# Optimization experiments

Measured on AMD Instinct MI355X. Metric: run time of the kernel, lower is better.

Reference implementation:

```python
import jax, jax.numpy as jnp
import numpy as np

D = 1024  # feature dim, power of two
B = 8192  # batch


def build_H(d):
    # scaled Hadamard matrix H with H @ H = I (since H is symmetric orthogonal)
    H = np.array([[1.0]], dtype=np.float32)
    while H.shape[0] < d:
        H = np.block([[H, H], [H, -H]])
    return jnp.asarray(H * d ** -0.5, dtype=jnp.float32)


def setup_inputs() -> dict:
    key = jax.random.key(0)
    ks = jax.random.split(key, 6)
    return {
        "x": jax.random.normal(ks[0], (B, D), jnp.float32),
        "s1": jax.random.normal(ks[1], (D,), jnp.float32),
        "s2": jax.random.normal(ks[2], (D,), jnp.float32),
        "mu": jax.random.normal(ks[3], (D,), jnp.float32),
        "Rho": jax.random.normal(ks[4], (D, D), jnp.float32),
        "epsilon": jax.random.normal(ks[5], (D,), jnp.float32),  # torch.randn(D) noise, hoisted
        "H": build_H(D),
    }


def _w_bar(s1, s2, u, H):
    # diag(s1) @ H @ diag(u) @ H @ diag(s2), via row/col scalings of H
    return ((s1[:, None] * H * u[None, :]) @ H) * s2[None, :]


def reference(x, s1, s2, mu, Rho, epsilon, H):
    r = jax.nn.softplus(Rho)
    sigma_sqrt = r @ r.T                      # [D, D]
    # w_bar is linear in u, so w_bar(mu) @ h + w_bar(sigma_sqrt @ eps) @ h
    # == w_bar(mu + sigma_sqrt @ eps) @ h  (same math, one GEMM chain)
    u = mu + sigma_sqrt @ epsilon             # [D]
    W = _w_bar(s1, s2, u, H)                  # [D, D]
    b = W @ x.T                               # [D, B]  (h = x.T as in the torch code)
    return jax.nn.relu(b)
```

## Files before the change

### kernel.cpp

```cpp
#include <hip/hip_runtime.h>
#include <math.h>

#define DD 1024
#define BB 8192

__device__ __forceinline__ float softplus_f(float x) {
    return fmaxf(x, 0.0f) + log1pf(expf(-fabsf(x)));
}

__global__ __launch_bounds__(256) void k_teps(const float* __restrict__ rho,
                                              const float* __restrict__ eps,
                                              float* __restrict__ t) {
    int j  = blockIdx.x * 256 + threadIdx.x;
    int i0 = blockIdx.y * 16;
    float acc = 0.f;
#pragma unroll
    for (int k = 0; k < 16; ++k) {
        int i = i0 + k;
        acc += softplus_f(rho[i * DD + j]) * eps[i];
    }
    atomicAdd(&t[j], acc);
}

__global__ __launch_bounds__(256) void k_u(const float* __restrict__ rho,
                                           const float* __restrict__ mu,
                                           const float* __restrict__ t,
                                           float* __restrict__ u) {
    int i  = blockIdx.x;
    int tx = threadIdx.x;
    float acc = 0.f;
#pragma unroll
    for (int c = 0; c < 4; ++c) {
        int j = tx + c * 256;
        acc += softplus_f(rho[i * DD + j]) * t[j];
    }
#pragma unroll
    for (int off = 32; off > 0; off >>= 1)
        acc += __shfl_down(acc, off, 64);
    __shared__ float red[4];
    int lane = tx & 63, w = tx >> 6;
    if (lane == 0) red[w] = acc;
    __syncthreads();
    if (tx == 0) u[i] = mu[i] + red[0] + red[1] + red[2] + red[3];
}


template <int CTRL>
__device__ __forceinline__ float dppmov(float x) {
    return __int_as_float(
        __builtin_amdgcn_mov_dpp(__float_as_int(x), CTRL, 0xF, 0xF, true));
}

__device__ __forceinline__ void fwht1024(float v[16], float sA, float sB,
                                         float sC, float sD, float sE, float sF) {
#pragma unroll
    for (int s = 1; s <= 8; s <<= 1) {
#pragma unroll
        for (int m = 0; m < 16; ++m)
            if ((m & s) == 0) {
                float a = v[m], b = v[m ^ s];
                v[m] = a + b;
                v[m ^ s] = a - b;
            }
    }
#pragma unroll
    for (int m = 0; m < 16; ++m) { float o = dppmov<0xB1>(v[m]);  v[m] = fmaf(v[m], sA, o); }
#pragma unroll
    for (int m = 0; m < 16; ++m) { float o = dppmov<0x4E>(v[m]);  v[m] = fmaf(v[m], sB, o); }
#pragma unroll
    for (int m = 0; m < 16; ++m) { float o = dppmov<0x141>(v[m]); v[m] = fmaf(v[m], sC, o); }
#pragma unroll
    for (int m = 0; m < 16; ++m) { float o = dppmov<0x140>(v[m]); v[m] = fmaf(v[m], sD, o); }
#pragma unroll
    for (int m = 0; m < 16; ++m) { float o = __shfl_xor(v[m], 16, 64); v[m] = fmaf(v[m], sE, o); }
#pragma unroll
    for (int m = 0; m < 16; ++m) { float o = __shfl_xor(v[m], 32, 64); v[m] = fmaf(v[m], sF, o); }
}

__global__ __launch_bounds__(512) void k_main(const float* __restrict__ x,
                                              const float* __restrict__ s1,
                                              const float* __restrict__ s2,
                                              const float* __restrict__ u,
                                              float* __restrict__ out) {
    __shared__ float tile[16 * 1024];
    const int t    = threadIdx.x;
    const int lane = t & 63;
    const int wv   = t >> 6;
    const int b0   = blockIdx.x * 16;

    const int l0 = lane & 1, l1 = (lane >> 1) & 1, l2 = (lane >> 2) & 1,
              l3 = (lane >> 3) & 1, l4 = (lane >> 4) & 1, l5 = (lane >> 5) & 1;
    const int hi = (l0 ^ l2) | ((l1 ^ l2) << 1) | ((l2 ^ l3) << 2) | (l3 << 3) |
                   (l4 << 4) | (l5 << 5);
    const int base = hi << 4;

    const float sA = (l0 ^ l2) ? -1.f : 1.f;
    const float sB = (l1 ^ l2) ? -1.f : 1.f;
    const float sC = (l2 ^ l3) ? -1.f : 1.f;
    const float sD = l3 ? -1.f : 1.f;
    const float sE = l4 ? -1.f : 1.f;
    const float sF = l5 ? -1.f : 1.f;

    float4 s2f[4], uf[4], s1f[4];
#pragma unroll
    for (int c = 0; c < 4; ++c) {
        s2f[c] = *(const float4*)(s2 + base + 4 * c);
        uf[c]  = *(const float4*)(u  + base + 4 * c);
        s1f[c] = *(const float4*)(s1 + base + 4 * c);
    }
    const int swz = (lane >> 1) & 15;

    for (int rr = 0; rr < 2; ++rr) {
        const int r = wv * 2 + rr;
        const float* xr = x + (b0 + r) * DD + base;
        float v[16];
#pragma unroll
        for (int c = 0; c < 4; ++c) {
            float4 xv = *(const float4*)(xr + 4 * c);
            v[4 * c + 0] = xv.x * s2f[c].x;
            v[4 * c + 1] = xv.y * s2f[c].y;
            v[4 * c + 2] = xv.z * s2f[c].z;
            v[4 * c + 3] = xv.w * s2f[c].w;
        }
        fwht1024(v, sA, sB, sC, sD, sE, sF);
#pragma unroll
        for (int c = 0; c < 4; ++c) {
            v[4 * c + 0] *= uf[c].x;
            v[4 * c + 1] *= uf[c].y;
            v[4 * c + 2] *= uf[c].z;
            v[4 * c + 3] *= uf[c].w;
        }
        fwht1024(v, sA, sB, sC, sD, sE, sF);
        const float kscale = 1.0f / 1024.0f;
        float* trow = tile + r * 1024 + base;
        const int sw2 = (swz ^ r) & 15;
#pragma unroll
        for (int c = 0; c < 4; ++c) {
            float y0 = fmaxf(v[4 * c + 0] * s1f[c].x * kscale, 0.f);
            float y1 = fmaxf(v[4 * c + 1] * s1f[c].y * kscale, 0.f);
            float y2 = fmaxf(v[4 * c + 2] * s1f[c].z * kscale, 0.f);
            float y3 = fmaxf(v[4 * c + 3] * s1f[c].w * kscale, 0.f);
            trow[(4 * c + 0) ^ sw2] = y0;
            trow[(4 * c + 1) ^ sw2] = y1;
            trow[(4 * c + 2) ^ sw2] = y2;
            trow[(4 * c + 3) ^ sw2] = y3;
        }
    }
    __syncthreads();

#pragma unroll
    for (int it = 0; it < 32; ++it) {
        int d = (t >> 4) + (it << 5);
        int r = t & 15;
        int h  = d >> 4;
        int h1 = (h >> 1) & 1, h2 = (h >> 2) & 1, h3 = (h >> 3) & 1,
            h4 = (h >> 4) & 1;
        int sw = (h1 ^ h2 ^ h3) | ((h2 ^ h3) << 1) | (h3 << 2) | (h4 << 3);
        float y = tile[r * 1024 + (d & ~15) + (((d & 15) ^ sw ^ r) & 15)];
        out[d * BB + b0 + r] = y;
    }
}

extern "C" void kernel_launch(void* const* d_in, const int* in_sizes, int n_in,
                              void* d_out, int out_size, void* d_ws, size_t ws_size,
                              hipStream_t stream) {
    const float* x   = (const float*)d_in[0];
    const float* s1  = (const float*)d_in[1];
    const float* s2  = (const float*)d_in[2];
    const float* mu  = (const float*)d_in[3];
    const float* rho = (const float*)d_in[4];
    const float* eps = (const float*)d_in[5];
    float* out = (float*)d_out;

    float* t = (float*)d_ws;
    float* u = t + DD;

    hipMemsetAsync(t, 0, DD * sizeof(float), stream);

    dim3 gA(4, 64);
    k_teps<<<gA, 256, 0, stream>>>(rho, eps, t);
    k_u<<<DD, 256, 0, stream>>>(rho, mu, t, u);
    k_main<<<BB / 16, 512, 0, stream>>>(x, s1, s2, u, out);
}
```

Baseline: 37.55 us.

## Vectorize transposed output stores, preload both rows, and drop atomics in t reduction

The transposed write-out now has each thread gather four batch rows from shared memory and emit one float4 store, replacing the scalar stores. The shared-tile layout gets an extra row-dependent XOR on the column block to keep bank conflicts down. Both rows' x loads are issued up front, and the 1/1024 scale is folded into s1. The t = softplus(Rho)^T eps step becomes a per-column block reduction with no memset and no atomics. That reduction reads Rho with a stride of one row per thread, which is uncoalesced and could make the small kernel slower.

```diff
diff --git a/kernel.cpp b/kernel.cpp
--- a/kernel.cpp
+++ b/kernel.cpp
@@ -8,18 +8,25 @@
     return fmaxf(x, 0.0f) + log1pf(expf(-fabsf(x)));
 }
 
-__global__ __launch_bounds__(256) void k_teps(const float* __restrict__ rho,
-                                              const float* __restrict__ eps,
-                                              float* __restrict__ t) {
-    int j  = blockIdx.x * 256 + threadIdx.x;
-    int i0 = blockIdx.y * 16;
+__global__ __launch_bounds__(256) void k_t(const float* __restrict__ rho,
+                                           const float* __restrict__ eps,
+                                           float* __restrict__ t) {
+    int j  = blockIdx.x;
+    int tx = threadIdx.x;
     float acc = 0.f;
 #pragma unroll
-    for (int k = 0; k < 16; ++k) {
-        int i = i0 + k;
+    for (int c = 0; c < 4; ++c) {
+        int i = tx + c * 256;
         acc += softplus_f(rho[i * DD + j]) * eps[i];
     }
-    atomicAdd(&t[j], acc);
+#pragma unroll
+    for (int off = 32; off > 0; off >>= 1)
+        acc += __shfl_down(acc, off, 64);
+    __shared__ float red[4];
+    int lane = tx & 63, w = tx >> 6;
+    if (lane == 0) red[w] = acc;
+    __syncthreads();
+    if (tx == 0) t[j] = red[0] + red[1] + red[2] + red[3];
 }
 
 __global__ __launch_bounds__(256) void k_u(const float* __restrict__ rho,
@@ -107,21 +114,31 @@
         s2f[c] = *(const float4*)(s2 + base + 4 * c);
         uf[c]  = *(const float4*)(u  + base + 4 * c);
         s1f[c] = *(const float4*)(s1 + base + 4 * c);
+        const float kscale = 1.0f / 1024.0f;
+        s1f[c].x *= kscale; s1f[c].y *= kscale;
+        s1f[c].z *= kscale; s1f[c].w *= kscale;
     }
     const int swz = (lane >> 1) & 15;
 
+    const int r0 = wv * 2;
+    const int r1 = r0 + 1;
+    const float* xr0 = x + (size_t)(b0 + r0) * DD + base;
+    const float* xr1 = xr0 + DD;
+    float va[16], vb[16];
+#pragma unroll
+    for (int c = 0; c < 4; ++c) {
+        float4 xv0 = *(const float4*)(xr0 + 4 * c);
+        float4 xv1 = *(const float4*)(xr1 + 4 * c);
+        va[4 * c + 0] = xv0.x * s2f[c].x;  vb[4 * c + 0] = xv1.x * s2f[c].x;
+        va[4 * c + 1] = xv0.y * s2f[c].y;  vb[4 * c + 1] = xv1.y * s2f[c].y;
+        va[4 * c + 2] = xv0.z * s2f[c].z;  vb[4 * c + 2] = xv1.z * s2f[c].z;
+        va[4 * c + 3] = xv0.w * s2f[c].w;  vb[4 * c + 3] = xv1.w * s2f[c].w;
+    }
+
+#pragma unroll
     for (int rr = 0; rr < 2; ++rr) {
-        const int r = wv * 2 + rr;
-        const float* xr = x + (b0 + r) * DD + base;
-        float v[16];
-#pragma unroll
-        for (int c = 0; c < 4; ++c) {
-            float4 xv = *(const float4*)(xr + 4 * c);
-            v[4 * c + 0] = xv.x * s2f[c].x;
-            v[4 * c + 1] = xv.y * s2f[c].y;
-            v[4 * c + 2] = xv.z * s2f[c].z;
-            v[4 * c + 3] = xv.w * s2f[c].w;
-        }
+        const int r = (rr == 0) ? r0 : r1;
+        float* v = (rr == 0) ? va : vb;
         fwht1024(v, sA, sB, sC, sD, sE, sF);
 #pragma unroll
         for (int c = 0; c < 4; ++c) {
@@ -131,33 +148,40 @@
             v[4 * c + 3] *= uf[c].w;
         }
         fwht1024(v, sA, sB, sC, sD, sE, sF);
-        const float kscale = 1.0f / 1024.0f;
-        float* trow = tile + r * 1024 + base;
+        float* trow = tile + r * 1024;
+        const int baseW = ((hi ^ ((r >> 2) & 3)) << 4);
         const int sw2 = (swz ^ r) & 15;
 #pragma unroll
         for (int c = 0; c < 4; ++c) {
-            float y0 = fmaxf(v[4 * c + 0] * s1f[c].x * kscale, 0.f);
-            float y1 = fmaxf(v[4 * c + 1] * s1f[c].y * kscale, 0.f);
-            float y2 = fmaxf(v[4 * c + 2] * s1f[c].z * kscale, 0.f);
-            float y3 = fmaxf(v[4 * c + 3] * s1f[c].w * kscale, 0.f);
-            trow[(4 * c + 0) ^ sw2] = y0;
-            trow[(4 * c + 1) ^ sw2] = y1;
-            trow[(4 * c + 2) ^ sw2] = y2;
-            trow[(4 * c + 3) ^ sw2] = y3;
+            float y0 = fmaxf(v[4 * c + 0] * s1f[c].x, 0.f);
+            float y1 = fmaxf(v[4 * c + 1] * s1f[c].y, 0.f);
+            float y2 = fmaxf(v[4 * c + 2] * s1f[c].z, 0.f);
+            float y3 = fmaxf(v[4 * c + 3] * s1f[c].w, 0.f);
+            trow[baseW + ((4 * c + 0) ^ sw2)] = y0;
+            trow[baseW + ((4 * c + 1) ^ sw2)] = y1;
+            trow[baseW + ((4 * c + 2) ^ sw2)] = y2;
+            trow[baseW + ((4 * c + 3) ^ sw2)] = y3;
         }
     }
     __syncthreads();
 
 #pragma unroll
-    for (int it = 0; it < 32; ++it) {
-        int d = (t >> 4) + (it << 5);
-        int r = t & 15;
-        int h  = d >> 4;
-        int h1 = (h >> 1) & 1, h2 = (h >> 2) & 1, h3 = (h >> 3) & 1,
-            h4 = (h >> 4) & 1;
-        int sw = (h1 ^ h2 ^ h3) | ((h2 ^ h3) << 1) | (h3 << 2) | (h4 << 3);
-        float y = tile[r * 1024 + (d & ~15) + (((d & 15) ^ sw ^ r) & 15)];
-        out[d * BB + b0 + r] = y;
+    for (int it = 0; it < 8; ++it) {
+        const int d  = (t >> 2) + (it << 7);
+        const int r4 = (t & 3) << 2;
+        const int q  = t & 3;
+        const int h  = d >> 4;
+        const int dl = d & 15;
+        const int h1 = (h >> 1) & 1, h2 = (h >> 2) & 1, h3 = (h >> 3) & 1,
+                  h4 = (h >> 4) & 1;
+        const int sw = (h1 ^ h2 ^ h3) | ((h2 ^ h3) << 1) | (h3 << 2) | (h4 << 3);
+        const int colhi = (h ^ q) << 4;
+        float4 y;
+        y.x = tile[(r4 + 0) * 1024 + colhi + ((dl ^ sw ^ (r4 + 0)) & 15)];
+        y.y = tile[(r4 + 1) * 1024 + colhi + ((dl ^ sw ^ (r4 + 1)) & 15)];
+        y.z = tile[(r4 + 2) * 1024 + colhi + ((dl ^ sw ^ (r4 + 2)) & 15)];
+        y.w = tile[(r4 + 3) * 1024 + colhi + ((dl ^ sw ^ (r4 + 3)) & 15)];
+        *(float4*)(out + (size_t)d * BB + b0 + r4) = y;
     }
 }
 
@@ -175,10 +199,7 @@
     float* t = (float*)d_ws;
     float* u = t + DD;
 
-    hipMemsetAsync(t, 0, DD * sizeof(float), stream);
-
-    dim3 gA(4, 64);
-    k_teps<<<gA, 256, 0, stream>>>(rho, eps, t);
+    k_t<<<DD, 256, 0, stream>>>(rho, eps, t);
     k_u<<<DD, 256, 0, stream>>>(rho, mu, t, u);
     k_main<<<BB / 16, 512, 0, stream>>>(x, s1, s2, u, out);
 }
```

After: 34.81 us. 1.08x faster.

## Replace atomic reduction with partial sums and vectorize transposed output stores

Applied to the files above, without the earlier changes.

The first stage no longer uses atomics and a memset. Each block reduces 64 rows in shared memory and writes per-column partial sums, which k_u then sums with float4 loads. In the main kernel the shared tile uses a new 16-float-group swizzle so that both the row writes and the transposed output writes go out as float4 instead of scalar stores. The 1/1024 scale is folded into s1, and launch bounds now request occupancy. This removes one launch and the atomic contention and cuts store instruction count, at the risk of new LDS bank conflicts from the swizzle.

```diff
diff --git a/kernel.cpp b/kernel.cpp
--- a/kernel.cpp
+++ b/kernel.cpp
@@ -8,23 +8,31 @@
     return fmaxf(x, 0.0f) + log1pf(expf(-fabsf(x)));
 }
 
-__global__ __launch_bounds__(256) void k_teps(const float* __restrict__ rho,
-                                              const float* __restrict__ eps,
-                                              float* __restrict__ t) {
-    int j  = blockIdx.x * 256 + threadIdx.x;
-    int i0 = blockIdx.y * 16;
+__global__ __launch_bounds__(256) void k_t(const float* __restrict__ rho,
+                                           const float* __restrict__ eps,
+                                           float* __restrict__ part) {
+    const int tx = threadIdx.x, lane = tx & 63, w = tx >> 6;
+    const int cg = blockIdx.x & 15, rg = blockIdx.x >> 4;
+    const int j = cg * 64 + lane;
+    const int rowbase = rg * 64 + w * 16;
     float acc = 0.f;
 #pragma unroll
     for (int k = 0; k < 16; ++k) {
-        int i = i0 + k;
-        acc += softplus_f(rho[i * DD + j]) * eps[i];
+        int row = rowbase + k;
+        acc += softplus_f(rho[row * DD + j]) * eps[row];
     }
-    atomicAdd(&t[j], acc);
+    __shared__ float red[4][64];
+    red[w][lane] = acc;
+    __syncthreads();
+    if (tx < 64) {
+        float s = red[0][tx] + red[1][tx] + red[2][tx] + red[3][tx];
+        part[(cg * 64 + tx) * 16 + rg] = s;
+    }
 }
 
 __global__ __launch_bounds__(256) void k_u(const float* __restrict__ rho,
                                            const float* __restrict__ mu,
-                                           const float* __restrict__ t,
+                                           const float* __restrict__ part,
                                            float* __restrict__ u) {
     int i  = blockIdx.x;
     int tx = threadIdx.x;
@@ -32,7 +40,11 @@
 #pragma unroll
     for (int c = 0; c < 4; ++c) {
         int j = tx + c * 256;
-        acc += softplus_f(rho[i * DD + j]) * t[j];
+        const float4* p4 = (const float4*)(part + j * 16);
+        float4 a = p4[0], b = p4[1], cc = p4[2], dd = p4[3];
+        float tj = ((a.x + a.y) + (a.z + a.w)) + ((b.x + b.y) + (b.z + b.w)) +
+                   ((cc.x + cc.y) + (cc.z + cc.w)) + ((dd.x + dd.y) + (dd.z + dd.w));
+        acc += softplus_f(rho[i * DD + j]) * tj;
     }
 #pragma unroll
     for (int off = 32; off > 0; off >>= 1)
@@ -77,12 +89,12 @@
     for (int m = 0; m < 16; ++m) { float o = __shfl_xor(v[m], 32, 64); v[m] = fmaf(v[m], sF, o); }
 }
 
-__global__ __launch_bounds__(512) void k_main(const float* __restrict__ x,
-                                              const float* __restrict__ s1,
-                                              const float* __restrict__ s2,
-                                              const float* __restrict__ u,
-                                              float* __restrict__ out) {
-    __shared__ float tile[16 * 1024];
+__global__ __launch_bounds__(512, 4) void k_main(const float* __restrict__ x,
+                                                 const float* __restrict__ s1,
+                                                 const float* __restrict__ s2,
+                                                 const float* __restrict__ u,
+                                                 float* __restrict__ out) {
+    __shared__ __align__(16) float tile[16 * 1024];
     const int t    = threadIdx.x;
     const int lane = t & 63;
     const int wv   = t >> 6;
@@ -107,12 +119,15 @@
         s2f[c] = *(const float4*)(s2 + base + 4 * c);
         uf[c]  = *(const float4*)(u  + base + 4 * c);
         s1f[c] = *(const float4*)(s1 + base + 4 * c);
+        const float kscale = 1.0f / 1024.0f;
+        s1f[c].x *= kscale; s1f[c].y *= kscale;
+        s1f[c].z *= kscale; s1f[c].w *= kscale;
     }
-    const int swz = (lane >> 1) & 15;
+    const int qsw = hi & 3;
 
     for (int rr = 0; rr < 2; ++rr) {
         const int r = wv * 2 + rr;
-        const float* xr = x + (b0 + r) * DD + base;
+        const float* xr = x + (size_t)(b0 + r) * DD + base;
         float v[16];
 #pragma unroll
         for (int c = 0; c < 4; ++c) {
@@ -131,33 +146,32 @@
             v[4 * c + 3] *= uf[c].w;
         }
         fwht1024(v, sA, sB, sC, sD, sE, sF);
-        const float kscale = 1.0f / 1024.0f;
-        float* trow = tile + r * 1024 + base;
-        const int sw2 = (swz ^ r) & 15;
+        float* trow = tile + r * 1024 + ((hi ^ ((r >> 2) & 3)) << 4);
 #pragma unroll
         for (int c = 0; c < 4; ++c) {
-            float y0 = fmaxf(v[4 * c + 0] * s1f[c].x * kscale, 0.f);
-            float y1 = fmaxf(v[4 * c + 1] * s1f[c].y * kscale, 0.f);
-            float y2 = fmaxf(v[4 * c + 2] * s1f[c].z * kscale, 0.f);
-            float y3 = fmaxf(v[4 * c + 3] * s1f[c].w * kscale, 0.f);
-            trow[(4 * c + 0) ^ sw2] = y0;
-            trow[(4 * c + 1) ^ sw2] = y1;
-            trow[(4 * c + 2) ^ sw2] = y2;
-            trow[(4 * c + 3) ^ sw2] = y3;
+            float4 y;
+            y.x = fmaxf(v[4 * c + 0] * s1f[c].x, 0.f);
+            y.y = fmaxf(v[4 * c + 1] * s1f[c].y, 0.f);
+            y.z = fmaxf(v[4 * c + 2] * s1f[c].z, 0.f);
+            y.w = fmaxf(v[4 * c + 3] * s1f[c].w, 0.f);
+            *(float4*)(trow + 4 * (c ^ qsw)) = y;
         }
     }
     __syncthreads();
 
 #pragma unroll
-    for (int it = 0; it < 32; ++it) {
-        int d = (t >> 4) + (it << 5);
-        int r = t & 15;
-        int h  = d >> 4;
-        int h1 = (h >> 1) & 1, h2 = (h >> 2) & 1, h3 = (h >> 3) & 1,
-            h4 = (h >> 4) & 1;
-        int sw = (h1 ^ h2 ^ h3) | ((h2 ^ h3) << 1) | (h3 << 2) | (h4 << 3);
-        float y = tile[r * 1024 + (d & ~15) + (((d & 15) ^ sw ^ r) & 15)];
-        out[d * BB + b0 + r] = y;
+    for (int it = 0; it < 8; ++it) {
+        const int d  = (t >> 2) + (it << 7);
+        const int r4 = (t & 3) << 2;
+        const int h  = d >> 4;
+        const int col = ((h ^ (t & 3)) << 4) + 4 * (((d >> 2) & 3) ^ (h & 3)) +
+                        (d & 3);
+        float4 y;
+        y.x = tile[(r4 + 0) * 1024 + col];
+        y.y = tile[(r4 + 1) * 1024 + col];
+        y.z = tile[(r4 + 2) * 1024 + col];
+        y.w = tile[(r4 + 3) * 1024 + col];
+        *(float4*)(out + (size_t)d * BB + b0 + r4) = y;
     }
 }
 
@@ -172,13 +186,10 @@
     const float* eps = (const float*)d_in[5];
     float* out = (float*)d_out;
 
-    float* t = (float*)d_ws;
-    float* u = t + DD;
+    float* part = (float*)d_ws;
+    float* u    = part + DD * 16;
 
-    hipMemsetAsync(t, 0, DD * sizeof(float), stream);
-
-    dim3 gA(4, 64);
-    k_teps<<<gA, 256, 0, stream>>>(rho, eps, t);
-    k_u<<<DD, 256, 0, stream>>>(rho, mu, t, u);
+    k_t<<<256, 256, 0, stream>>>(rho, eps, part);
+    k_u<<<DD, 256, 0, stream>>>(rho, mu, part, u);
     k_main<<<BB / 16, 512, 0, stream>>>(x, s1, s2, u, out);
 }
```

New measurement: 34.79 us. 7.3% less time.
